# Performance work log

Hardware: AMD Instinct MI355X
Metric: run time of the kernel (lower is better)

## Reference

```python
import jax, jax.numpy as jnp
import numpy as np

# Constants from init_kwargs: XGate(s=1, index=3, dim=3, N=14)
S = 1        # shift amount of the X gate
INDEX = 3    # which qudit the gate acts on
DIM = 3      # qudit dimension
NQ = 14      # number of qudits
BATCH = 8    # number of state vectors (columns of x)

D = DIM ** NQ                    # full Hilbert-space dimension = 4,782,969
L = DIM ** INDEX                 # left identity block size
R = DIM ** (NQ - INDEX - 1)      # right identity block size


def setup_inputs() -> dict:
    key = jax.random.key(0)
    x = jax.random.normal(key, (D, BATCH), dtype=jnp.float32)
    return {"x": x}


def reference(x):
    # U = I_L kron M kron I_R, with M[j, i] = delta(j, (i + S) % DIM).
    # (U @ x)[j] picks x[i] where i = (j - S) % DIM on the INDEX-th qudit axis,
    # i.e. a cyclic roll by S along that axis. This is the exact math of the
    # sparse permutation matmul, expressed as a strided gather.
    b = x.shape[1]
    xr = x.reshape(L, DIM, R, b)           # split out the acted-on qudit axis
    out = jnp.roll(xr, S, axis=1)          # out[..., j, ...] = x[..., (j-S)%DIM, ...]
    return out.reshape(D, b)
```

## Files before the change

### kernel.cpp

```cpp
#include <hip/hip_runtime.h>


typedef float f4 __attribute__((ext_vector_type(4)));

constexpr int DIMQ    = 3;
constexpr int LBLK    = 27;
constexpr int RBLK    = 59049;
constexpr int BATCH   = 8;
constexpr int CHUNK_F = RBLK * BATCH;
constexpr int CHUNK_V = CHUNK_F / 4;
constexpr int NCHUNK  = LBLK * DIMQ;

constexpr int BLOCK  = 256;
constexpr int UNROLL = 4;
constexpr int TILE   = BLOCK * UNROLL;
constexpr int GX     = (CHUNK_V + TILE - 1) / TILE;

__global__ __launch_bounds__(BLOCK) void xgate_roll_kernel(
        const f4* __restrict__ in, f4* __restrict__ out) {
    const int chunk = blockIdx.y;
    const int j = chunk % 3;
    const int dst_base = chunk * CHUNK_V;
    const int src_base = dst_base + (j == 0 ? 2 * CHUNK_V : -CHUNK_V);

    const int v0 = blockIdx.x * TILE + (int)threadIdx.x;

    if (v0 + (UNROLL - 1) * BLOCK < CHUNK_V) {
        f4 r[UNROLL];
#pragma unroll
        for (int k = 0; k < UNROLL; ++k)
            r[k] = in[src_base + v0 + k * BLOCK];
#pragma unroll
        for (int k = 0; k < UNROLL; ++k)
            out[dst_base + v0 + k * BLOCK] = r[k];
    } else {
#pragma unroll
        for (int k = 0; k < UNROLL; ++k) {
            const int v = v0 + k * BLOCK;
            if (v < CHUNK_V) {
                out[dst_base + v] = in[src_base + v];
            }
        }
    }
}

extern "C" void kernel_launch(void* const* d_in, const int* in_sizes, int n_in,
                              void* d_out, int out_size, void* d_ws, size_t ws_size,
                              hipStream_t stream) {
    const f4* x = (const f4*)d_in[0];
    f4* out = (f4*)d_out;
    dim3 block(BLOCK);
    dim3 grid(GX, NCHUNK);
    xgate_roll_kernel<<<grid, block, 0, stream>>>(x, out);
}
```

Measured before the change: 261.8 us.

## Use grid-stride pipelined copy loop with nontemporal loads and stores

Shrinks the x-dimension of the grid to a fixed 24 blocks per chunk. Each thread now walks its chunk with a grid stride, loading the next tile while storing the previous one, which hides memory latency in software. All global loads and stores become nontemporal so the streamed data bypasses cache retention. The trade-off is fewer resident blocks to hide latency, plus more complex tail handling.

```diff
diff --git a/kernel.cpp b/kernel.cpp
--- a/kernel.cpp
+++ b/kernel.cpp
@@ -14,7 +14,8 @@
 constexpr int BLOCK  = 256;
 constexpr int UNROLL = 4;
 constexpr int TILE   = BLOCK * UNROLL;
-constexpr int GX     = (CHUNK_V + TILE - 1) / TILE;
+constexpr int GX     = 24;
+constexpr int STRIDE = GX * TILE;
 
 __global__ __launch_bounds__(BLOCK) void xgate_roll_kernel(
         const f4* __restrict__ in, f4* __restrict__ out) {
@@ -23,23 +24,41 @@
     const int dst_base = chunk * CHUNK_V;
     const int src_base = dst_base + (j == 0 ? 2 * CHUNK_V : -CHUNK_V);
 
-    const int v0 = blockIdx.x * TILE + (int)threadIdx.x;
+    int v = blockIdx.x * TILE + (int)threadIdx.x;
 
-    if (v0 + (UNROLL - 1) * BLOCK < CHUNK_V) {
+    if (v + (UNROLL - 1) * BLOCK < CHUNK_V) {
         f4 r[UNROLL];
 #pragma unroll
         for (int k = 0; k < UNROLL; ++k)
-            r[k] = in[src_base + v0 + k * BLOCK];
+            r[k] = __builtin_nontemporal_load(&in[src_base + v + k * BLOCK]);
+
+        int vn = v + STRIDE;
+        while (vn + (UNROLL - 1) * BLOCK < CHUNK_V) {
+            f4 s[UNROLL];
+#pragma unroll
+            for (int k = 0; k < UNROLL; ++k)
+                s[k] = __builtin_nontemporal_load(&in[src_base + vn + k * BLOCK]);
+#pragma unroll
+            for (int k = 0; k < UNROLL; ++k)
+                __builtin_nontemporal_store(r[k], &out[dst_base + v + k * BLOCK]);
+#pragma unroll
+            for (int k = 0; k < UNROLL; ++k)
+                r[k] = s[k];
+            v = vn;
+            vn += STRIDE;
+        }
 #pragma unroll
         for (int k = 0; k < UNROLL; ++k)
-            out[dst_base + v0 + k * BLOCK] = r[k];
-    } else {
+            __builtin_nontemporal_store(r[k], &out[dst_base + v + k * BLOCK]);
+        v = vn;
+    }
+
 #pragma unroll
-        for (int k = 0; k < UNROLL; ++k) {
-            const int v = v0 + k * BLOCK;
-            if (v < CHUNK_V) {
-                out[dst_base + v] = in[src_base + v];
-            }
+    for (int k = 0; k < UNROLL; ++k) {
+        const int vv = v + k * BLOCK;
+        if (vv < CHUNK_V) {
+            f4 r = __builtin_nontemporal_load(&in[src_base + vv]);
+            __builtin_nontemporal_store(r, &out[dst_base + vv]);
         }
     }
 }
```

Result: no change. 260.7 us (-0.4%).
